# Optimization experiments

Hardware: AMD Instinct MI355X
Metric: run time of the kernel (lower is better)

The kernel has to match this reference:

```python
import jax, jax.numpy as jnp
import numpy as np

N = 100000      # nodes
E = 1600000     # edges (avg degree 16)
DIN = 128
DOUT = 128


def setup_inputs() -> dict:
    key = jax.random.key(0)
    k1, k2, k3, k4 = jax.random.split(key, 4)
    x = jax.random.normal(k1, (N, DIN), dtype=jnp.float32)
    edge_index = jax.random.randint(k2, (2, E), 0, N, dtype=jnp.int64)
    # guarantee every node appears at least once as a source row so that
    # degree > 0 everywhere (1/sqrt(0) would be inf, as in the torch code)
    row = edge_index[0].at[:N].set(jnp.arange(N, dtype=jnp.int64))
    edge_index = jnp.stack([row, edge_index[1]])
    W = jax.random.normal(k3, (DOUT, DIN), dtype=jnp.float32) / np.sqrt(DIN)
    b = jax.random.normal(k4, (DOUT,), dtype=jnp.float32) * 0.01
    return {"x": x, "edge_index": edge_index, "W": W, "b": b}


def reference(x, edge_index, W, b):
    # Math identical to: A = dense(add_self_loops(edge_index));
    # D = 1/sqrt(degree(edge_index[0]))  (degree WITHOUT self-loops);
    # out = (D_i * A_ij * D_j) @ (x W^T + b)
    row, col = edge_index[0], edge_index[1]
    deg = jax.ops.segment_sum(jnp.ones(row.shape[0], x.dtype), row, num_segments=N)
    d = jax.lax.rsqrt(deg)                      # [N]
    h = x @ W.T + b                             # [N, DOUT]
    # edge contributions: out[r] += D[r] * D[c] * h[c]  (duplicate edges sum, as to_dense does)
    agg = jax.ops.segment_sum(d[col][:, None] * h[col], row, num_segments=N)
    # self-loop term added for every node: D[i]^2 * h[i]
    out = d[:, None] * agg + (d * d)[:, None] * h
    return out
```

## Files before the change

### kernel.cpp

```cpp
#include <hip/hip_runtime.h>

#define D 128
#define BROWS 1024
#define CAP 17408
#define CHUNK 2048

typedef __attribute__((ext_vector_type(8))) short bf16x8;
typedef __attribute__((ext_vector_type(4))) float f32x4;

__device__ inline unsigned short f2bf(float f) {
    unsigned u = __float_as_uint(f);
    u += 0x7FFFu + ((u >> 16) & 1u);
    return (unsigned short)(u >> 16);
}
__device__ inline float bf2f(unsigned short h) {
    return __uint_as_float((unsigned)h << 16);
}
__device__ inline float bflo(unsigned u) { return __uint_as_float(u << 16); }
__device__ inline float bfhi(unsigned u) { return __uint_as_float(u & 0xFFFF0000u); }

__global__ __launch_bounds__(256) void k_bin(const int* __restrict__ row,
                                             const int* __restrict__ col,
                                             int E, int* __restrict__ gcur,
                                             unsigned* __restrict__ ebuf) {
    __shared__ int lhist[128];
    __shared__ int sc[128];
    __shared__ int gbase[128];
    __shared__ unsigned sstage[CHUNK];
    __shared__ int sdest[CHUNK];
    int t = threadIdx.x;
    int base = blockIdx.x * CHUNK;
    if (t < 128) lhist[t] = 0;
    __syncthreads();
    int b[8], p[8]; unsigned pk[8];
    #pragma unroll
    for (int i = 0; i < 8; ++i) {
        int idx = base + i * 256 + t;
        if (idx < E) {
            int r = row[idx], c = col[idx];
            b[i] = r >> 10;
            pk[i] = ((unsigned)(r & (BROWS - 1)) << 17) | (unsigned)c;
            p[i] = atomicAdd(&lhist[b[i]], 1);
        } else b[i] = -1;
    }
    __syncthreads();
    if (t < 64) {
        int a0 = lhist[2 * t], a1 = lhist[2 * t + 1];
        int s = a0 + a1;
        int incl = s;
        #pragma unroll
        for (int m = 1; m < 64; m <<= 1) {
            int tmp = __shfl_up(incl, m);
            if (t >= m) incl += tmp;
        }
        int excl = incl - s;
        sc[2 * t] = excl;
        sc[2 * t + 1] = excl + a0;
        if (a0 > 0) gbase[2 * t] = atomicAdd(&gcur[2 * t], a0);
        if (a1 > 0) gbase[2 * t + 1] = atomicAdd(&gcur[2 * t + 1], a1);
    }
    __syncthreads();
    #pragma unroll
    for (int i = 0; i < 8; ++i) {
        if (b[i] >= 0) {
            int lidx = sc[b[i]] + p[i];
            int rel = gbase[b[i]] + p[i];
            sstage[lidx] = pk[i];
            sdest[lidx] = (rel < CAP) ? (b[i] * CAP + rel) : -1;
        }
    }
    __syncthreads();
    int total = sc[127] + lhist[127];
    for (int i = t; i < total; i += 256) {
        int d = sdest[i];
        if (d >= 0) ebuf[d] = sstage[i];
    }
}

__global__ __launch_bounds__(1024) void k_bdeg(const int* __restrict__ gcur,
                                               const unsigned* __restrict__ ebuf,
                                               int N, float* __restrict__ dvals,
                                               int* __restrict__ rscan) {
    __shared__ int lhist[1024];
    __shared__ int wtot[16];
    __shared__ int woff[16];
    int bkt = blockIdx.x, t = threadIdx.x;
    int cnt = gcur[bkt]; if (cnt > CAP) cnt = CAP;
    lhist[t] = 0;
    __syncthreads();
    const unsigned* ep = ebuf + (size_t)bkt * CAP;
    for (int i = t; i < cnt; i += 1024)
        atomicAdd(&lhist[ep[i] >> 17], 1);
    __syncthreads();
    int v = lhist[t];
    int lane = t & 63, wv = t >> 6;
    int incl = v;
    #pragma unroll
    for (int m = 1; m < 64; m <<= 1) {
        int tmp = __shfl_up(incl, m);
        if (lane >= m) incl += tmp;
    }
    if (lane == 63) wtot[wv] = incl;
    __syncthreads();
    if (t < 16) {
        int w = wtot[t];
        int wincl = w;
        #pragma unroll
        for (int m = 1; m < 16; m <<= 1) {
            int tmp = __shfl_up(wincl, m);
            if (t >= m) wincl += tmp;
        }
        woff[t] = wincl - w;
    }
    __syncthreads();
    int r = (bkt << 10) + t;
    if (r < N) {
        rscan[r] = woff[wv] + incl - v;
        dvals[r] = rsqrtf((float)v);
    }
}

__global__ __launch_bounds__(1024) void k_sort(const int* __restrict__ gcur,
                                               const unsigned* __restrict__ ebuf,
                                               const int* __restrict__ rscan,
                                               int N, int E, int NBK,
                                               int* __restrict__ rptr,
                                               int* __restrict__ csr_col) {
    __shared__ int lcur[1024];
    __shared__ int sebase;
    int bkt = blockIdx.x, t = threadIdx.x;
    int cnt = gcur[bkt]; if (cnt > CAP) cnt = CAP;
    if (t < 64) {
        int acc = 0;
        for (int i = t; i < bkt; i += 64) {
            int g = gcur[i];
            acc += (g > CAP) ? CAP : g;
        }
        #pragma unroll
        for (int m = 1; m < 64; m <<= 1) acc += __shfl_xor(acc, m);
        if (t == 0) sebase = acc;
    }
    int r = (bkt << 10) + t;
    int rel = (r < N) ? rscan[r] : 0;
    lcur[t] = rel;
    __syncthreads();
    int ebase = sebase;
    if (r < N) rptr[r] = ebase + rel;
    if (bkt == NBK - 1 && t == 0) rptr[N] = ebase + cnt;
    const unsigned* ep = ebuf + (size_t)bkt * CAP;
    for (int i = t; i < cnt; i += 1024) {
        unsigned e = ep[i];
        int rr = (int)(e >> 17);
        int p = atomicAdd(&lcur[rr], 1);
        csr_col[ebase + p] = (int)(e & 0x1FFFFu);
    }
}

__global__ void k_cast(const float* __restrict__ x, const float* __restrict__ dvals,
                       unsigned short* __restrict__ xs, int total4) {
    int i = blockIdx.x * blockDim.x + threadIdx.x;
    if (i >= total4) return;
    float4 v = ((const float4*)x)[i];
    float d = dvals[i >> 5];
    ushort4 o = make_ushort4(f2bf(d * v.x), f2bf(d * v.y), f2bf(d * v.z), f2bf(d * v.w));
    ((ushort4*)xs)[i] = o;
}

__global__ __launch_bounds__(256) void k_rows(const unsigned short* __restrict__ xs,
                                              const int* __restrict__ rptr,
                                              const int* __restrict__ csr_col,
                                              const float* __restrict__ dvals,
                                              float* __restrict__ ssum,
                                              float* __restrict__ y, int N) {
    int wid = (blockIdx.x * blockDim.x + threadIdx.x) >> 6;
    if (wid >= N) return;
    int lane = threadIdx.x & 63;
    int grp = lane >> 4, sl = lane & 15;
    int s = rptr[wid];
    int n = rptr[wid + 1] - s;
    float a[8] = {0.f, 0.f, 0.f, 0.f, 0.f, 0.f, 0.f, 0.f};
    float sumd = 0.f;
    const uint4* xsv = (const uint4*)xs;
    for (int k0 = 0; k0 < n; k0 += 4) {
        int idx = k0 + grp;
        if (idx < n) {
            int cc = csr_col[s + idx];
            uint4 v = xsv[cc * 16 + sl];
            sumd += dvals[cc];
            a[0] += bflo(v.x); a[1] += bfhi(v.x);
            a[2] += bflo(v.y); a[3] += bfhi(v.y);
            a[4] += bflo(v.z); a[5] += bfhi(v.z);
            a[6] += bflo(v.w); a[7] += bfhi(v.w);
        }
    }
    if (grp == 0) {
        uint4 v = xsv[wid * 16 + sl];
        a[0] += bflo(v.x); a[1] += bfhi(v.x);
        a[2] += bflo(v.y); a[3] += bfhi(v.y);
        a[4] += bflo(v.z); a[5] += bfhi(v.z);
        a[6] += bflo(v.w); a[7] += bfhi(v.w);
    }
    #pragma unroll
    for (int j = 0; j < 8; ++j) {
        a[j] += __shfl_xor(a[j], 16);
        a[j] += __shfl_xor(a[j], 32);
    }
    sumd += __shfl_xor(sumd, 16);
    sumd += __shfl_xor(sumd, 32);
    float dr = dvals[wid];
    if (grp < 2) {
        float4 o = (grp == 0) ? make_float4(a[0], a[1], a[2], a[3])
                              : make_float4(a[4], a[5], a[6], a[7]);
        o.x *= dr; o.y *= dr; o.z *= dr; o.w *= dr;
        ((float4*)(y + (size_t)wid * D))[sl * 2 + grp] = o;
    }
    if (lane == 0) ssum[wid] = dr * (dr + sumd);
}

#define LDSW 136

__global__ __launch_bounds__(256, 2) void k_gemm(const float* __restrict__ W,
                                                 const float* __restrict__ b,
                                                 const float* __restrict__ ssum,
                                                 float* yo, int N) {
    __shared__ unsigned short Whi[128 * LDSW];
    __shared__ unsigned short Wlo[128 * LDSW];
    __shared__ float bs[D];
    int t = threadIdx.x;
    #pragma unroll
    for (int i = 0; i < 16; ++i) {
        int idx4 = i * 256 + t;
        float4 w4 = ((const float4*)W)[idx4];
        int r = idx4 >> 5;
        int c = (idx4 & 31) * 4;
        unsigned short h0 = f2bf(w4.x), h1 = f2bf(w4.y), h2 = f2bf(w4.z), h3 = f2bf(w4.w);
        unsigned short l0 = f2bf(w4.x - bf2f(h0));
        unsigned short l1 = f2bf(w4.y - bf2f(h1));
        unsigned short l2 = f2bf(w4.z - bf2f(h2));
        unsigned short l3 = f2bf(w4.w - bf2f(h3));
        ushort4* ph = (ushort4*)&Whi[r * LDSW + c];
        ushort4* pl = (ushort4*)&Wlo[r * LDSW + c];
        *ph = make_ushort4(h0, h1, h2, h3);
        *pl = make_ushort4(l0, l1, l2, l3);
    }
    if (t < D) bs[t] = b[t];
    __syncthreads();

    int wave = t >> 6, lane = t & 63;
    int quad = lane >> 4, mrow = lane & 15;
    int row_base = blockIdx.x * 128 + wave * 32;

    bf16x8 Ahi[2][4], Alo[2][4];
    #pragma unroll
    for (int s = 0; s < 2; ++s) {
        int grow = row_base + s * 16 + mrow;
        bool ok = grow < N;
        const float* yrow = yo + (size_t)(ok ? grow : 0) * D;
        #pragma unroll
        for (int kk = 0; kk < 4; ++kk) {
            int k0 = kk * 32 + quad * 8;
            float4 f0 = ok ? ((const float4*)(yrow + k0))[0] : make_float4(0, 0, 0, 0);
            float4 f1 = ok ? ((const float4*)(yrow + k0))[1] : make_float4(0, 0, 0, 0);
            float fv[8] = {f0.x, f0.y, f0.z, f0.w, f1.x, f1.y, f1.z, f1.w};
            #pragma unroll
            for (int j = 0; j < 8; ++j) {
                unsigned short h = f2bf(fv[j]);
                Ahi[s][kk][j] = (short)h;
                Alo[s][kk][j] = (short)f2bf(fv[j] - bf2f(h));
            }
        }
    }

    f32x4 acc[2][8];
    #pragma unroll
    for (int s = 0; s < 2; ++s)
        #pragma unroll
        for (int ct = 0; ct < 8; ++ct)
            acc[s][ct] = (f32x4){0.f, 0.f, 0.f, 0.f};

    #pragma unroll
    for (int ct = 0; ct < 8; ++ct) {
        int wrow = ct * 16 + mrow;
        #pragma unroll
        for (int kk = 0; kk < 4; ++kk) {
            int off = wrow * LDSW + kk * 32 + quad * 8;
            bf16x8 Bhi = *(const bf16x8*)&Whi[off];
            bf16x8 Blo = *(const bf16x8*)&Wlo[off];
            #pragma unroll
            for (int s = 0; s < 2; ++s) {
                acc[s][ct] = __builtin_amdgcn_mfma_f32_16x16x32_bf16(Ahi[s][kk], Bhi, acc[s][ct], 0, 0, 0);
                acc[s][ct] = __builtin_amdgcn_mfma_f32_16x16x32_bf16(Alo[s][kk], Bhi, acc[s][ct], 0, 0, 0);
                acc[s][ct] = __builtin_amdgcn_mfma_f32_16x16x32_bf16(Ahi[s][kk], Blo, acc[s][ct], 0, 0, 0);
            }
        }
    }

    #pragma unroll
    for (int s = 0; s < 2; ++s) {
        #pragma unroll
        for (int r = 0; r < 4; ++r) {
            int grow = row_base + s * 16 + quad * 4 + r;
            if (grow < N) {
                float sv = ssum[grow];
                #pragma unroll
                for (int ct = 0; ct < 8; ++ct) {
                    int col = ct * 16 + mrow;
                    yo[(size_t)grow * D + col] = acc[s][ct][r] + sv * bs[col];
                }
            }
        }
    }
}

extern "C" void kernel_launch(void* const* d_in, const int* in_sizes, int n_in,
                              void* d_out, int out_size, void* d_ws, size_t ws_size,
                              hipStream_t stream) {
    const float* x  = (const float*)d_in[0];
    const int*   ei = (const int*)d_in[1];
    const float* W  = (const float*)d_in[2];
    const float* b  = (const float*)d_in[3];
    float* out = (float*)d_out;
    int N = in_sizes[0] / D;
    int E = in_sizes[1] / 2;
    int NBK = (N + BROWS - 1) / BROWS;
    int NCH = (E + CHUNK - 1) / CHUNK;

    int*      gcur    = (int*)d_ws;
    int*      rscan   = gcur + 128;
    int*      rptr    = rscan + N;
    float*    dvals   = (float*)(rptr + N + 1);
    float*    ssum    = dvals + N;
    int*      csr_col = (int*)(ssum + N);
    unsigned* ebuf    = (unsigned*)(csr_col + E);
    uintptr_t xs_addr = (uintptr_t)(ebuf + (size_t)NBK * CAP);
    xs_addr = (xs_addr + 15) & ~(uintptr_t)15;
    unsigned short* xs = (unsigned short*)xs_addr;

    hipMemsetAsync(gcur, 0, 128 * sizeof(int), stream);
    k_bin<<<NCH, 256, 0, stream>>>(ei, ei + E, E, gcur, ebuf);
    k_bdeg<<<NBK, 1024, 0, stream>>>(gcur, ebuf, N, dvals, rscan);
    k_sort<<<NBK, 1024, 0, stream>>>(gcur, ebuf, rscan, N, E, NBK, rptr, csr_col);
    k_cast<<<(N * (D / 4) + 255) / 256, 256, 0, stream>>>(x, dvals, xs, N * (D / 4));
    k_rows<<<(N + 3) / 4, 256, 0, stream>>>(xs, rptr, csr_col, dvals, ssum, out, N);
    k_gemm<<<(N + 127) / 128, 256, 0, stream>>>(W, b, ssum, out, N);
}
```

Before: 286.0 us.

## Count degrees with global atomics in binning, merge deg and sort kernels, unroll gather

Row degrees are now counted with global atomicAdd in k_bin, so the separate k_bdeg pass that histogrammed each bucket from ebuf is removed. The scan and the CSR scatter are merged into one k_build kernel, which drops one launch and the rscan round trip. The row-gather loop in k_rows now loads two neighbours per group per iteration, putting more loads in flight. The cost is 1.6M global atomics spread over 100K addresses and a larger memset covering the degree array.

```diff
diff --git a/kernel.cpp b/kernel.cpp
--- a/kernel.cpp
+++ b/kernel.cpp
@@ -22,6 +22,7 @@
 __global__ __launch_bounds__(256) void k_bin(const int* __restrict__ row,
                                              const int* __restrict__ col,
                                              int E, int* __restrict__ gcur,
+                                             int* __restrict__ deg,
                                              unsigned* __restrict__ ebuf) {
     __shared__ int lhist[128];
     __shared__ int sc[128];
@@ -41,6 +42,7 @@
             b[i] = r >> 10;
             pk[i] = ((unsigned)(r & (BROWS - 1)) << 17) | (unsigned)c;
             p[i] = atomicAdd(&lhist[b[i]], 1);
+            atomicAdd(&deg[r], 1);
         } else b[i] = -1;
     }
     __syncthreads();
@@ -77,22 +79,21 @@
     }
 }
 
-__global__ __launch_bounds__(1024) void k_bdeg(const int* __restrict__ gcur,
-                                               const unsigned* __restrict__ ebuf,
-                                               int N, float* __restrict__ dvals,
-                                               int* __restrict__ rscan) {
-    __shared__ int lhist[1024];
+__global__ __launch_bounds__(1024) void k_build(const int* __restrict__ gcur,
+                                                const int* __restrict__ deg,
+                                                const unsigned* __restrict__ ebuf,
+                                                int N, int NBK,
+                                                int* __restrict__ rptr,
+                                                float* __restrict__ dvals,
+                                                int* __restrict__ csr_col) {
+    __shared__ int lcur[1024];
     __shared__ int wtot[16];
     __shared__ int woff[16];
+    __shared__ int sebase;
     int bkt = blockIdx.x, t = threadIdx.x;
     int cnt = gcur[bkt]; if (cnt > CAP) cnt = CAP;
-    lhist[t] = 0;
-    __syncthreads();
-    const unsigned* ep = ebuf + (size_t)bkt * CAP;
-    for (int i = t; i < cnt; i += 1024)
-        atomicAdd(&lhist[ep[i] >> 17], 1);
-    __syncthreads();
-    int v = lhist[t];
+    int r = (bkt << 10) + t;
+    int v = (r < N) ? deg[r] : 0;
     int lane = t & 63, wv = t >> 6;
     int incl = v;
     #pragma unroll
@@ -111,42 +112,27 @@
             if (t >= m) wincl += tmp;
         }
         woff[t] = wincl - w;
-    }
-    __syncthreads();
-    int r = (bkt << 10) + t;
-    if (r < N) {
-        rscan[r] = woff[wv] + incl - v;
-        dvals[r] = rsqrtf((float)v);
-    }
-}
-
-__global__ __launch_bounds__(1024) void k_sort(const int* __restrict__ gcur,
-                                               const unsigned* __restrict__ ebuf,
-                                               const int* __restrict__ rscan,
-                                               int N, int E, int NBK,
-                                               int* __restrict__ rptr,
-                                               int* __restrict__ csr_col) {
-    __shared__ int lcur[1024];
-    __shared__ int sebase;
-    int bkt = blockIdx.x, t = threadIdx.x;
-    int cnt = gcur[bkt]; if (cnt > CAP) cnt = CAP;
-    if (t < 64) {
+    } else if (t >= 64 && t < 128) {
+        int tt = t - 64;
         int acc = 0;
-        for (int i = t; i < bkt; i += 64) {
+        for (int i = tt; i < bkt; i += 64) {
             int g = gcur[i];
             acc += (g > CAP) ? CAP : g;
         }
         #pragma unroll
         for (int m = 1; m < 64; m <<= 1) acc += __shfl_xor(acc, m);
-        if (t == 0) sebase = acc;
-    }
-    int r = (bkt << 10) + t;
-    int rel = (r < N) ? rscan[r] : 0;
+        if (tt == 0) sebase = acc;
+    }
+    __syncthreads();
+    int rel = woff[wv] + incl - v;
+    int ebase = sebase;
+    if (r < N) {
+        rptr[r] = ebase + rel;
+        dvals[r] = rsqrtf((float)v);
+    }
+    if (bkt == NBK - 1 && t == 0) rptr[N] = ebase + cnt;
     lcur[t] = rel;
     __syncthreads();
-    int ebase = sebase;
-    if (r < N) rptr[r] = ebase + rel;
-    if (bkt == NBK - 1 && t == 0) rptr[N] = ebase + cnt;
     const unsigned* ep = ebuf + (size_t)bkt * CAP;
     for (int i = t; i < cnt; i += 1024) {
         unsigned e = ep[i];
@@ -181,17 +167,24 @@
     float a[8] = {0.f, 0.f, 0.f, 0.f, 0.f, 0.f, 0.f, 0.f};
     float sumd = 0.f;
     const uint4* xsv = (const uint4*)xs;
-    for (int k0 = 0; k0 < n; k0 += 4) {
-        int idx = k0 + grp;
-        if (idx < n) {
-            int cc = csr_col[s + idx];
-            uint4 v = xsv[cc * 16 + sl];
-            sumd += dvals[cc];
-            a[0] += bflo(v.x); a[1] += bfhi(v.x);
-            a[2] += bflo(v.y); a[3] += bfhi(v.y);
-            a[4] += bflo(v.z); a[5] += bfhi(v.z);
-            a[6] += bflo(v.w); a[7] += bfhi(v.w);
-        }
+    for (int k0 = 0; k0 < n; k0 += 8) {
+        int i0 = k0 + grp, i1 = k0 + 4 + grp;
+        bool g0 = i0 < n, g1 = i1 < n;
+        int c0 = g0 ? csr_col[s + i0] : 0;
+        int c1 = g1 ? csr_col[s + i1] : 0;
+        uint4 v0 = {0, 0, 0, 0}, v1 = {0, 0, 0, 0};
+        float d0 = 0.f, d1 = 0.f;
+        if (g0) { v0 = xsv[c0 * 16 + sl]; d0 = dvals[c0]; }
+        if (g1) { v1 = xsv[c1 * 16 + sl]; d1 = dvals[c1]; }
+        sumd += d0 + d1;
+        a[0] += bflo(v0.x); a[1] += bfhi(v0.x);
+        a[2] += bflo(v0.y); a[3] += bfhi(v0.y);
+        a[4] += bflo(v0.z); a[5] += bfhi(v0.z);
+        a[6] += bflo(v0.w); a[7] += bfhi(v0.w);
+        a[0] += bflo(v1.x); a[1] += bfhi(v1.x);
+        a[2] += bflo(v1.y); a[3] += bfhi(v1.y);
+        a[4] += bflo(v1.z); a[5] += bfhi(v1.z);
+        a[6] += bflo(v1.w); a[7] += bfhi(v1.w);
     }
     if (grp == 0) {
         uint4 v = xsv[wid * 16 + sl];
@@ -326,8 +319,8 @@
     int NCH = (E + CHUNK - 1) / CHUNK;
 
     int*      gcur    = (int*)d_ws;
-    int*      rscan   = gcur + 128;
-    int*      rptr    = rscan + N;
+    int*      deg     = gcur + 128;
+    int*      rptr    = deg + N;
     float*    dvals   = (float*)(rptr + N + 1);
     float*    ssum    = dvals + N;
     int*      csr_col = (int*)(ssum + N);
@@ -336,10 +329,9 @@
     xs_addr = (xs_addr + 15) & ~(uintptr_t)15;
     unsigned short* xs = (unsigned short*)xs_addr;
 
-    hipMemsetAsync(gcur, 0, 128 * sizeof(int), stream);
-    k_bin<<<NCH, 256, 0, stream>>>(ei, ei + E, E, gcur, ebuf);
-    k_bdeg<<<NBK, 1024, 0, stream>>>(gcur, ebuf, N, dvals, rscan);
-    k_sort<<<NBK, 1024, 0, stream>>>(gcur, ebuf, rscan, N, E, NBK, rptr, csr_col);
+    hipMemsetAsync(gcur, 0, (size_t)(128 + N) * sizeof(int), stream);
+    k_bin<<<NCH, 256, 0, stream>>>(ei, ei + E, E, gcur, deg, ebuf);
+    k_build<<<NBK, 1024, 0, stream>>>(gcur, deg, ebuf, N, NBK, rptr, dvals, csr_col);
     k_cast<<<(N * (D / 4) + 255) / 256, 256, 0, stream>>>(x, dvals, xs, N * (D / 4));
     k_rows<<<(N + 3) / 4, 256, 0, stream>>>(xs, rptr, csr_col, dvals, ssum, out, N);
     k_gemm<<<(N + 127) / 128, 256, 0, stream>>>(W, b, ssum, out, N);
```

Measured after the change: 336.2 us. 1.18x slower.
